# Kernel optimization log

Measured on AMD Instinct MI355X. Metric: run time of the kernel, lower is better.

## Reference

```python
import jax, jax.numpy as jnp
import numpy as np

B, T, C, M = 32, 720, 862, 4
PRED, LABEL = 720, 48
D, H, FF, LAYERS = 512, 8, 2048, 3
E = D // H
LN_EPS = 1e-5
REVIN_EPS = 1e-5


def _ln(x, w, b):
    mu = jnp.mean(x, axis=-1, keepdims=True)
    var = jnp.var(x, axis=-1, keepdims=True)
    return (x - mu) * jax.lax.rsqrt(var + LN_EPS) * w + b


def _flow_attention(q, k, v):
    # q, k, v: [B, H, L, E]. Flowformer: sigmoid kernel + flow conservation
    # (incoming/outgoing normalizers), competition (sigmoid) and allocation (softmax).
    q = jax.nn.sigmoid(q)
    k = jax.nn.sigmoid(k)
    eps = 1e-6
    Lq, Ls = q.shape[2], k.shape[2]
    nr = 1.0 / jnp.einsum('bhld,bhd->bhl', q + eps, k.sum(2) + eps)          # sink incoming
    nc = 1.0 / jnp.einsum('bhsd,bhd->bhs', k + eps, q.sum(2) + eps)          # source outgoing
    nr_ref = jnp.einsum('bhld,bhd->bhl', q + eps, (k * nc[..., None]).sum(2) + eps)
    nc_ref = jnp.einsum('bhsd,bhd->bhs', k + eps, (q * nr[..., None]).sum(2) + eps)
    nr_ref = jax.nn.sigmoid(nr_ref * (float(Lq) / float(Ls)))                # competition
    nc_ref = jax.nn.softmax(nc_ref, axis=-1) * Ls                            # allocation
    kv = jnp.einsum('bhse,bhsd->bhed', k, v * nc_ref[..., None])             # [B,H,E,E]
    return jnp.einsum('bhle,bhed->bhld', q, kv) * (nr * nr_ref)[..., None]


def _forward(x_enc, x_mark_enc, x_dec, revin_w, revin_b, emb_W, emb_b,
             Wq, bq, Wk, bk, Wv, bv, Wo, bo,
             ff1_W, ff1_b, ff2_W, ff2_b,
             ln1_w, ln1_b, ln2_w, ln2_b, lnf_w, lnf_b, proj_W, proj_b):
    # RevIN 'norm': per-channel instance norm over time + affine
    mean = jnp.mean(x_enc, axis=1, keepdims=True)
    stdev = jnp.sqrt(jnp.var(x_enc, axis=1, keepdims=True) + REVIN_EPS)
    xn = (x_enc - mean) / stdev * revin_w + revin_b
    # inverted embedding: each channel / covariate series -> one d_model token
    tok = jnp.concatenate([xn.transpose(0, 2, 1), x_mark_enc.transpose(0, 2, 1)], axis=1)  # [B, C+M, T]
    x = tok @ emb_W + emb_b  # [B, C+M, D]
    Ltok = x.shape[1]
    for l in range(LAYERS):
        q = (x @ Wq[l] + bq[l]).reshape(B, Ltok, H, E).transpose(0, 2, 1, 3)
        k = (x @ Wk[l] + bk[l]).reshape(B, Ltok, H, E).transpose(0, 2, 1, 3)
        v = (x @ Wv[l] + bv[l]).reshape(B, Ltok, H, E).transpose(0, 2, 1, 3)
        a = _flow_attention(q, k, v).transpose(0, 2, 1, 3).reshape(B, Ltok, D)
        x = _ln(x + (a @ Wo[l] + bo[l]), ln1_w[l], ln1_b[l])
        y = jax.nn.gelu(x @ ff1_W[l] + ff1_b[l], approximate=False)
        x = _ln(x + (y @ ff2_W[l] + ff2_b[l]), ln2_w[l], ln2_b[l])
    x = _ln(x, lnf_w, lnf_b)
    out = (x @ proj_W + proj_b).transpose(0, 2, 1)[:, :, :x_dec.shape[-1]]  # [B, PRED, C]
    # RevIN 'denorm'
    out = (out - revin_b) / (revin_w + REVIN_EPS * REVIN_EPS)
    out = out * stdev + mean
    return out[:, -PRED:, :]


def setup_inputs() -> dict:
    key = jax.random.key(0)
    ks = iter(jax.random.split(key, 40))

    def rn(shape, scale=0.02):
        return (jax.random.normal(next(ks), shape, jnp.float32) * scale)

    return {
        'x_enc': jax.random.normal(next(ks), (B, T, C), jnp.float32),
        'x_mark_enc': jax.random.normal(next(ks), (B, T, M), jnp.float32),
        'x_dec': jax.random.normal(next(ks), (B, LABEL + PRED, C), jnp.float32),
        'x_mark_dec': jax.random.normal(next(ks), (B, LABEL + PRED, M), jnp.float32),
        'revin_w': jnp.ones((C,), jnp.float32),
        'revin_b': jnp.zeros((C,), jnp.float32),
        'emb_W': rn((T, D)), 'emb_b': jnp.zeros((D,), jnp.float32),
        'Wq': rn((LAYERS, D, D)), 'bq': jnp.zeros((LAYERS, D), jnp.float32),
        'Wk': rn((LAYERS, D, D)), 'bk': jnp.zeros((LAYERS, D), jnp.float32),
        'Wv': rn((LAYERS, D, D)), 'bv': jnp.zeros((LAYERS, D), jnp.float32),
        'Wo': rn((LAYERS, D, D)), 'bo': jnp.zeros((LAYERS, D), jnp.float32),
        'ff1_W': rn((LAYERS, D, FF)), 'ff1_b': jnp.zeros((LAYERS, FF), jnp.float32),
        'ff2_W': rn((LAYERS, FF, D)), 'ff2_b': jnp.zeros((LAYERS, D), jnp.float32),
        'ln1_w': jnp.ones((LAYERS, D), jnp.float32), 'ln1_b': jnp.zeros((LAYERS, D), jnp.float32),
        'ln2_w': jnp.ones((LAYERS, D), jnp.float32), 'ln2_b': jnp.zeros((LAYERS, D), jnp.float32),
        'lnf_w': jnp.ones((D,), jnp.float32), 'lnf_b': jnp.zeros((D,), jnp.float32),
        'proj_W': rn((D, PRED)), 'proj_b': jnp.zeros((PRED,), jnp.float32),
    }


def reference(x_enc, x_mark_enc, x_dec, x_mark_dec, revin_w, revin_b, emb_W, emb_b,
              Wq, bq, Wk, bk, Wv, bv, Wo, bo,
              ff1_W, ff1_b, ff2_W, ff2_b,
              ln1_w, ln1_b, ln2_w, ln2_b, lnf_w, lnf_b, proj_W, proj_b):
    return _forward(x_enc, x_mark_enc, x_dec, revin_w, revin_b, emb_W, emb_b,
                    Wq, bq, Wk, bk, Wv, bv, Wo, bo,
                    ff1_W, ff1_b, ff2_W, ff2_b,
                    ln1_w, ln1_b, ln2_w, ln2_b, lnf_w, lnf_b, proj_W, proj_b)
```

## Files before the change

### kernel.cpp

```cpp
#include <hip/hip_runtime.h>
#include <math.h>

#define BB 32
#define TT 720
#define CC 862
#define MM 4
#define LTOK 866
#define DD 512
#define HH 8
#define EE 64
#define FFD 2048
#define NTOK (BB * LTOK)
#define NBH (BB * HH)
#define KPAD 736
#define NPADP 768
#define LSPLIT 4
#define LCHUNK 224
#define KVSPLIT 8
#define KVCHUNK 112
#define QS 1536
#define TSPL 8
#define TCH 90
#define CSLD 136

typedef unsigned short ushort_t;
typedef short s8v __attribute__((ext_vector_type(8)));
typedef float f4v __attribute__((ext_vector_type(4)));

__device__ __forceinline__ float wave_sum(float v) {
    #pragma unroll
    for (int off = 32; off; off >>= 1) v += __shfl_xor(v, off, 64);
    return v;
}
__device__ __forceinline__ float b2f(ushort_t u) {
    return __uint_as_float(((unsigned int)u) << 16);
}
__device__ __forceinline__ ushort_t f2b(float f) {
    unsigned int u = __float_as_uint(f);
    u = (u + 0x7FFFu + ((u >> 16) & 1u)) >> 16;
    return (ushort_t)u;
}

__device__ __forceinline__ void xcd_tile(int gx, int* m_t, int* n_t) {
    int nwg = gx * gridDim.y;
    int bid = blockIdx.y * gx + blockIdx.x;
    int xcd = bid & 7;
    int lid = bid >> 3;
    int q = nwg >> 3, r = nwg & 7;
    int wgid = (xcd < r ? xcd * (q + 1) : r * (q + 1) + (xcd - r) * q) + lid;
    *m_t = wgid / gx;
    *n_t = wgid % gx;
}

__global__ __launch_bounds__(256) void revin_part(const float* __restrict__ x_enc,
                                                  float* __restrict__ pS,
                                                  float* __restrict__ pS2) {
    int b = blockIdx.y, tz = blockIdx.z;
    int c = blockIdx.x * 64 + (threadIdx.x & 63);
    int g = threadIdx.x >> 6;
    float s = 0.f, s2 = 0.f;
    if (c < CC) {
        int t0 = tz * TCH;
        for (int t = t0 + g; t < t0 + TCH; t += 4) {
            float v = x_enc[((size_t)b * TT + t) * CC + c];
            s += v; s2 += v * v;
        }
    }
    __shared__ float ls[4][64], ls2[4][64];
    ls[g][threadIdx.x & 63] = s; ls2[g][threadIdx.x & 63] = s2;
    __syncthreads();
    if (g == 0 && c < CC) {
        int cx = threadIdx.x & 63;
        s = ls[0][cx] + ls[1][cx] + ls[2][cx] + ls[3][cx];
        s2 = ls2[0][cx] + ls2[1][cx] + ls2[2][cx] + ls2[3][cx];
        pS[((size_t)tz * BB + b) * CC + c] = s;
        pS2[((size_t)tz * BB + b) * CC + c] = s2;
    }
}

__global__ __launch_bounds__(256) void revin_fin(const float* __restrict__ pS,
                                                 const float* __restrict__ pS2,
                                                 float* __restrict__ mean,
                                                 float* __restrict__ stdev) {
    int idx = blockIdx.x * 256 + threadIdx.x;
    if (idx >= BB * CC) return;
    float s = 0.f, s2 = 0.f;
    #pragma unroll
    for (int tz = 0; tz < TSPL; tz++) {
        s += pS[(size_t)tz * BB * CC + idx];
        s2 += pS2[(size_t)tz * BB * CC + idx];
    }
    float mu = s / (float)TT;
    float var = s2 / (float)TT - mu * mu;
    mean[idx] = mu;
    stdev[idx] = sqrtf(var + 1e-5f);
}

__global__ __launch_bounds__(256) void build_tok(const float* __restrict__ x_enc,
                                                 const float* __restrict__ x_mark,
                                                 const float* __restrict__ mean,
                                                 const float* __restrict__ stdev,
                                                 const float* __restrict__ rw,
                                                 const float* __restrict__ rb,
                                                 ushort_t* __restrict__ tok) {
    int b = blockIdx.z;
    int r0 = blockIdx.x * 32, t0 = blockIdx.y * 32;
    __shared__ float tile[32][33];
    int tx = threadIdx.x & 31, ty = threadIdx.x >> 5;
    #pragma unroll
    for (int kk = 0; kk < 4; kk++) {
        int t = t0 + ty + kk * 8, r = r0 + tx;
        float v = 0.f;
        if (t < TT && r < LTOK) {
            if (r < CC) {
                float xv = x_enc[((size_t)b * TT + t) * CC + r];
                v = (xv - mean[b * CC + r]) / stdev[b * CC + r] * rw[r] + rb[r];
            } else {
                v = x_mark[((size_t)b * TT + t) * MM + (r - CC)];
            }
        }
        tile[ty + kk * 8][tx] = v;
    }
    __syncthreads();
    #pragma unroll
    for (int kk = 0; kk < 4; kk++) {
        int r = r0 + ty + kk * 8, t = t0 + tx;
        if (r < LTOK && t < KPAD)
            tok[((size_t)b * LTOK + r) * KPAD + t] = f2b(tile[tx][ty + kk * 8]);
    }
}

__global__ __launch_bounds__(256) void convT(const float* __restrict__ W,
                                             ushort_t* __restrict__ Wt,
                                             int K, int N, int KP, int NP) {
    __shared__ float tile[32][33];
    int k0 = blockIdx.x * 32, n0 = blockIdx.y * 32;
    int tx = threadIdx.x & 31, ty = threadIdx.x >> 5;
    #pragma unroll
    for (int r = 0; r < 4; r++) {
        int k = k0 + ty + r * 8, n = n0 + tx;
        tile[ty + r * 8][tx] = (k < K && n < N) ? W[(size_t)k * N + n] : 0.f;
    }
    __syncthreads();
    #pragma unroll
    for (int r = 0; r < 4; r++) {
        int n = n0 + ty + r * 8, k = k0 + tx;
        if (n < NP && k < KP)
            Wt[(size_t)n * KP + k] = f2b(tile[tx][ty + r * 8]);
    }
}

#define GLL(g, l) __builtin_amdgcn_global_load_lds( \
    (const __attribute__((address_space(1))) void*)(g), \
    (__attribute__((address_space(3))) void*)(l), 16, 0, 0)

template <int ACT, bool OF, bool OB>
__global__ __launch_bounds__(256) void bgemm(const ushort_t* __restrict__ A,
                                             const ushort_t* __restrict__ Bt,
                                             const float* __restrict__ bias,
                                             float* __restrict__ Cf,
                                             ushort_t* __restrict__ Cb,
                                             int Mdim, int Kdim, int Nout) {
    __shared__ ushort_t smem[17408];
    ushort_t* As = smem;
    ushort_t* Bs = smem + 4096;
    const int tid = threadIdx.x;
    const int lane = tid & 63;
    const int wid = tid >> 6;
    int m_t, n_t;
    xcd_tile(gridDim.x, &m_t, &n_t);
    const int m0 = m_t * 128;
    const int n0 = n_t * 128;
    const int wm = wid & 1, wn = wid >> 1;

    f4v acc[4][4];
    #pragma unroll
    for (int i = 0; i < 4; i++)
        #pragma unroll
        for (int j = 0; j < 4; j++)
            acc[i][j] = (f4v){0.f, 0.f, 0.f, 0.f};

    const int srow = wid * 16 + (lane >> 2);
    const int skq = ((lane & 3) ^ ((lane >> 3) & 3)) * 8;
    int ar0 = m0 + srow;       if (ar0 > Mdim - 1) ar0 = Mdim - 1;
    int ar1 = m0 + 64 + srow;  if (ar1 > Mdim - 1) ar1 = Mdim - 1;
    const ushort_t* gA0 = A + (size_t)ar0 * Kdim + skq;
    const ushort_t* gA1 = A + (size_t)ar1 * Kdim + skq;
    const ushort_t* gB0 = Bt + (size_t)(n0 + srow) * Kdim + skq;
    const ushort_t* gB1 = Bt + (size_t)(n0 + 64 + srow) * Kdim + skq;
    ushort_t* lA0 = As + (wid * 16) * 32;
    ushort_t* lA1 = As + (64 + wid * 16) * 32;
    ushort_t* lB0 = Bs + (wid * 16) * 32;
    ushort_t* lB1 = Bs + (64 + wid * 16) * 32;

    const int lr = lane & 15;
    const int kc = (((lane >> 4) ^ ((lane >> 1) & 3))) * 8;

    for (int k0 = 0; k0 < Kdim; k0 += 32) {
        GLL(gA0 + k0, lA0);
        GLL(gA1 + k0, lA1);
        GLL(gB0 + k0, lB0);
        GLL(gB1 + k0, lB1);
        __syncthreads();
        s8v af[4], bf[4];
        #pragma unroll
        for (int i = 0; i < 4; i++)
            af[i] = *(const s8v*)&As[(wm * 64 + i * 16 + lr) * 32 + kc];
        #pragma unroll
        for (int j = 0; j < 4; j++)
            bf[j] = *(const s8v*)&Bs[(wn * 64 + j * 16 + lr) * 32 + kc];
        #pragma unroll
        for (int i = 0; i < 4; i++)
            #pragma unroll
            for (int j = 0; j < 4; j++)
                acc[i][j] = __builtin_amdgcn_mfma_f32_16x16x32_bf16(af[i], bf[j], acc[i][j], 0, 0, 0);
        __syncthreads();
    }

    const int orow = (lane >> 4) * 4;
    if (OF) {
        #pragma unroll
        for (int j = 0; j < 4; j++) {
            int col = n0 + wn * 64 + j * 16 + lr;
            bool cok = col < Nout;
            float bb = cok ? bias[col] : 0.f;
            #pragma unroll
            for (int i = 0; i < 4; i++) {
                #pragma unroll
                for (int r = 0; r < 4; r++) {
                    int row = m0 + wm * 64 + i * 16 + orow + r;
                    if (cok && row < Mdim) {
                        float v = acc[i][j][r] + bb;
                        if (ACT == 1) v = 0.5f * v * (1.0f + erff(v * 0.70710678118654752f));
                        if (ACT == 2) v = 1.0f / (1.0f + expf(-v));
                        Cf[(size_t)row * Nout + col] = v;
                    }
                }
            }
        }
    }
    if (OB) {
        #pragma unroll
        for (int j = 0; j < 4; j++) {
            int cl = wn * 64 + j * 16 + lr;
            int gcol = n0 + cl;
            float bb = (gcol < Nout) ? bias[gcol] : 0.f;
            #pragma unroll
            for (int i = 0; i < 4; i++) {
                #pragma unroll
                for (int r = 0; r < 4; r++) {
                    float v = acc[i][j][r] + bb;
                    if (ACT == 1) v = 0.5f * v * (1.0f + erff(v * 0.70710678118654752f));
                    if (ACT == 2) v = 1.0f / (1.0f + expf(-v));
                    smem[(wm * 64 + i * 16 + orow + r) * CSLD + cl] = f2b(v);
                }
            }
        }
        __syncthreads();
        #pragma unroll
        for (int c = 0; c < 8; c++) {
            int idx = c * 256 + tid;
            int row = idx >> 4, cs = idx & 15;
            int grow = m0 + row, gcol = n0 + cs * 8;
            if (grow < Mdim) {
                if (gcol + 8 <= Nout) {
                    *(s8v*)&Cb[(size_t)grow * Nout + gcol] = *(const s8v*)&smem[row * CSLD + cs * 8];
                } else if (gcol < Nout) {
                    for (int q = 0; q < Nout - gcol; q++)
                        Cb[(size_t)grow * Nout + gcol + q] = smem[row * CSLD + cs * 8 + q];
                }
            }
        }
    }
}

__global__ __launch_bounds__(256) void bgemm_qkv(const ushort_t* __restrict__ A,
                                                 const ushort_t* __restrict__ Bt,
                                                 const float* __restrict__ bq_,
                                                 const float* __restrict__ bk_,
                                                 const float* __restrict__ bv_,
                                                 ushort_t* __restrict__ Cb,
                                                 int Mdim) {
    __shared__ ushort_t smem[17408];
    ushort_t* As = smem;
    ushort_t* Bs = smem + 4096;
    const int tid = threadIdx.x;
    const int lane = tid & 63;
    const int wid = tid >> 6;
    int m_t, n_t;
    xcd_tile(gridDim.x, &m_t, &n_t);
    const int m0 = m_t * 128;
    const int n0 = n_t * 128;
    const int wm = wid & 1, wn = wid >> 1;

    f4v acc[4][4];
    #pragma unroll
    for (int i = 0; i < 4; i++)
        #pragma unroll
        for (int j = 0; j < 4; j++)
            acc[i][j] = (f4v){0.f, 0.f, 0.f, 0.f};

    const int srow = wid * 16 + (lane >> 2);
    const int skq = ((lane & 3) ^ ((lane >> 3) & 3)) * 8;
    int ar0 = m0 + srow;       if (ar0 > Mdim - 1) ar0 = Mdim - 1;
    int ar1 = m0 + 64 + srow;  if (ar1 > Mdim - 1) ar1 = Mdim - 1;
    const ushort_t* gA0 = A + (size_t)ar0 * DD + skq;
    const ushort_t* gA1 = A + (size_t)ar1 * DD + skq;
    const ushort_t* gB0 = Bt + (size_t)(n0 + srow) * DD + skq;
    const ushort_t* gB1 = Bt + (size_t)(n0 + 64 + srow) * DD + skq;
    ushort_t* lA0 = As + (wid * 16) * 32;
    ushort_t* lA1 = As + (64 + wid * 16) * 32;
    ushort_t* lB0 = Bs + (wid * 16) * 32;
    ushort_t* lB1 = Bs + (64 + wid * 16) * 32;

    const int lr = lane & 15;
    const int kc = (((lane >> 4) ^ ((lane >> 1) & 3))) * 8;

    for (int k0 = 0; k0 < DD; k0 += 32) {
        GLL(gA0 + k0, lA0);
        GLL(gA1 + k0, lA1);
        GLL(gB0 + k0, lB0);
        GLL(gB1 + k0, lB1);
        __syncthreads();
        s8v af[4], bf[4];
        #pragma unroll
        for (int i = 0; i < 4; i++)
            af[i] = *(const s8v*)&As[(wm * 64 + i * 16 + lr) * 32 + kc];
        #pragma unroll
        for (int j = 0; j < 4; j++)
            bf[j] = *(const s8v*)&Bs[(wn * 64 + j * 16 + lr) * 32 + kc];
        #pragma unroll
        for (int i = 0; i < 4; i++)
            #pragma unroll
            for (int j = 0; j < 4; j++)
                acc[i][j] = __builtin_amdgcn_mfma_f32_16x16x32_bf16(af[i], bf[j], acc[i][j], 0, 0, 0);
        __syncthreads();
    }

    const int orow = (lane >> 4) * 4;
    #pragma unroll
    for (int j = 0; j < 4; j++) {
        int cl = wn * 64 + j * 16 + lr;
        int col = n0 + cl;
        int sec = col >> 9;
        const float* bsel = (sec == 0) ? bq_ : ((sec == 1) ? bk_ : bv_);
        float bb = bsel[col & 511];
        #pragma unroll
        for (int i = 0; i < 4; i++) {
            #pragma unroll
            for (int r = 0; r < 4; r++) {
                float v = acc[i][j][r] + bb;
                if (sec < 2) v = 1.0f / (1.0f + expf(-v));
                smem[(wm * 64 + i * 16 + orow + r) * CSLD + cl] = f2b(v);
            }
        }
    }
    __syncthreads();
    #pragma unroll
    for (int c = 0; c < 8; c++) {
        int idx = c * 256 + tid;
        int row = idx >> 4, cs = idx & 15;
        int grow = m0 + row;
        if (grow < Mdim)
            *(s8v*)&Cb[(size_t)grow * QS + n0 + cs * 8] = *(const s8v*)&smem[row * CSLD + cs * 8];
    }
}

__global__ __launch_bounds__(256) void ln_kernel(float* __restrict__ x,
                                                 const ushort_t* __restrict__ res,
                                                 const float* __restrict__ w,
                                                 const float* __restrict__ bp,
                                                 ushort_t* __restrict__ xb) {
    size_t base = (size_t)blockIdx.x * DD;
    int tid = threadIdx.x;
    float v0 = x[base + tid];
    float v1 = x[base + tid + 256];
    if (res != nullptr) { v0 += b2f(res[base + tid]); v1 += b2f(res[base + tid + 256]); }
    float s = wave_sum(v0 + v1);
    float s2 = wave_sum(v0 * v0 + v1 * v1);
    __shared__ float a1[4], a2[4];
    if ((tid & 63) == 0) { a1[tid >> 6] = s; a2[tid >> 6] = s2; }
    __syncthreads();
    s = a1[0] + a1[1] + a1[2] + a1[3];
    s2 = a2[0] + a2[1] + a2[2] + a2[3];
    float mu = s * (1.0f / DD);
    float var = s2 * (1.0f / DD) - mu * mu;
    float rs = rsqrtf(var + 1e-5f);
    float o0 = (v0 - mu) * rs * w[tid] + bp[tid];
    float o1 = (v1 - mu) * rs * w[tid + 256] + bp[tid + 256];
    x[base + tid] = o0;
    x[base + tid + 256] = o1;
    xb[base + tid] = f2b(o0);
    xb[base + tid + 256] = f2b(o1);
}

template <bool WEIGHTED>
__global__ __launch_bounds__(256) void attn_sums(const ushort_t* __restrict__ Q,
                                                 const ushort_t* __restrict__ Kp,
                                                 const float* __restrict__ wq,
                                                 const float* __restrict__ wk,
                                                 float* __restrict__ qsumP,
                                                 float* __restrict__ ksumP) {
    int bh = blockIdx.x;
    int sp = blockIdx.y;
    int b = bh >> 3, h = bh & 7;
    int lane = threadIdx.x & 63, g = threadIdx.x >> 6;
    int eo = (lane & 7) * 8;
    int lofs = lane >> 3;
    const size_t base = ((size_t)b * LTOK) * QS + h * 64 + eo;
    float aq[8] = {}, ak[8] = {};
    int lend = sp * LCHUNK + LCHUNK; if (lend > LTOK) lend = LTOK;
    for (int l = sp * LCHUNK + g * 8 + lofs; l < lend; l += 32) {
        s8v q8 = *(const s8v*)&Q[base + (size_t)l * QS];
        s8v k8 = *(const s8v*)&Kp[base + (size_t)l * QS];
        float wqv = 1.f, wkv = 1.f;
        if (WEIGHTED) { wqv = wq[bh * LTOK + l]; wkv = wk[bh * LTOK + l]; }
        #pragma unroll
        for (int j = 0; j < 8; j++) {
            aq[j] += b2f((ushort_t)q8[j]) * wqv;
            ak[j] += b2f((ushort_t)k8[j]) * wkv;
        }
    }
    #pragma unroll
    for (int off = 8; off < 64; off <<= 1) {
        #pragma unroll
        for (int j = 0; j < 8; j++) {
            aq[j] += __shfl_xor(aq[j], off, 64);
            ak[j] += __shfl_xor(ak[j], off, 64);
        }
    }
    __shared__ float sqs[4][64], sks[4][64];
    if (lofs == 0) {
        #pragma unroll
        for (int j = 0; j < 8; j++) { sqs[g][eo + j] = aq[j]; sks[g][eo + j] = ak[j]; }
    }
    __syncthreads();
    if (threadIdx.x < 64) {
        int e = threadIdx.x;
        float fq = sqs[0][e] + sqs[1][e] + sqs[2][e] + sqs[3][e];
        float fk = sks[0][e] + sks[1][e] + sks[2][e] + sks[3][e];
        qsumP[((size_t)sp * NBH + bh) * 64 + e] = fq;
        ksumP[((size_t)sp * NBH + bh) * 64 + e] = fk;
    }
}

template <int MODE>
__global__ __launch_bounds__(256) void attn_dots(const ushort_t* __restrict__ Q,
                                                 const ushort_t* __restrict__ Kp,
                                                 const float* __restrict__ Sq,
                                                 const float* __restrict__ Sk,
                                                 float* __restrict__ outq,
                                                 float* __restrict__ outk) {
    int bh = blockIdx.x;
    int b = bh >> 3, h = bh & 7;
    int lane = threadIdx.x & 63, w = threadIdx.x >> 6;
    float sq = 0.f, sk = 0.f;
    #pragma unroll
    for (int sp = 0; sp < LSPLIT; sp++) {
        sq += Sq[((size_t)sp * NBH + bh) * 64 + lane];
        sk += Sk[((size_t)sp * NBH + bh) * 64 + lane];
    }
    sq += 1e-6f; sk += 1e-6f;
    const size_t base = ((size_t)b * LTOK) * QS + h * 64 + lane;
    int l0 = blockIdx.y * 64 + w * 16;
    for (int i = 0; i < 16; i++) {
        int l = l0 + i;
        if (l >= LTOK) break;
        float dq = (b2f(Q[base + (size_t)l * QS]) + 1e-6f) * sq;
        float dk = (b2f(Kp[base + (size_t)l * QS]) + 1e-6f) * sk;
        dq = wave_sum(dq);
        dk = wave_sum(dk);
        if (lane == 0) {
            if (MODE == 0) { outq[bh * LTOK + l] = 1.0f / dq; outk[bh * LTOK + l] = 1.0f / dk; }
            else { outq[bh * LTOK + l] = 1.0f / (1.0f + expf(-dq)); outk[bh * LTOK + l] = dk; }
        }
    }
}

__global__ __launch_bounds__(256) void attn_softmax(float* __restrict__ buf) {
    float* p = buf + (size_t)blockIdx.x * LTOK;
    int tid = threadIdx.x;
    __shared__ float red[4];
    float mx = -1e30f;
    for (int l = tid; l < LTOK; l += 256) mx = fmaxf(mx, p[l]);
    #pragma unroll
    for (int off = 32; off; off >>= 1) mx = fmaxf(mx, __shfl_xor(mx, off, 64));
    if ((tid & 63) == 0) red[tid >> 6] = mx;
    __syncthreads();
    mx = fmaxf(fmaxf(red[0], red[1]), fmaxf(red[2], red[3]));
    __syncthreads();
    float s = 0.f;
    for (int l = tid; l < LTOK; l += 256) s += expf(p[l] - mx);
    s = wave_sum(s);
    if ((tid & 63) == 0) red[tid >> 6] = s;
    __syncthreads();
    s = red[0] + red[1] + red[2] + red[3];
    float scale = (float)LTOK / s;
    for (int l = tid; l < LTOK; l += 256) p[l] = expf(p[l] - mx) * scale;
}

__global__ __launch_bounds__(256) void attn_kv_part(const ushort_t* __restrict__ Kp,
                                                    const ushort_t* __restrict__ V,
                                                    const float* __restrict__ ncref,
                                                    float* __restrict__ kvpart) {
    int bh = blockIdx.x;
    int sp = blockIdx.y;
    int b = bh >> 3, h = bh & 7;
    int d = threadIdx.x & 63, eg = threadIdx.x >> 6;
    __shared__ float ks[16][64], vs[16][64];
    float acc[16] = {};
    const size_t base = ((size_t)b * LTOK) * QS + h * 64;
    const int s_begin = sp * KVCHUNK;
    int s_end = s_begin + KVCHUNK; if (s_end > LTOK) s_end = LTOK;

    const bool isV = threadIdx.x >= 128;
    const int slot = threadIdx.x & 127;
    const int srow = slot >> 3;
    const int e0 = (slot & 7) * 8;
    const ushort_t* src = isV ? V : Kp;

    for (int s0 = s_begin; s0 < s_end; s0 += 16) {
        __syncthreads();
        int s = s0 + srow;
        float vals[8] = {};
        if (s < s_end) {
            s8v raw = *(const s8v*)&src[base + (size_t)s * QS + e0];
            float mul = isV ? ncref[bh * LTOK + s] : 1.f;
            #pragma unroll
            for (int j = 0; j < 8; j++) vals[j] = b2f((ushort_t)raw[j]) * mul;
        }
        float (*dst)[64] = isV ? vs : ks;
        #pragma unroll
        for (int j = 0; j < 8; j++) dst[srow][e0 + j] = vals[j];
        __syncthreads();
        int nsi = s_end - s0; if (nsi > 16) nsi = 16;
        for (int si = 0; si < nsi; si++) {
            float vv = vs[si][d];
            #pragma unroll
            for (int i = 0; i < 16; i++) acc[i] += ks[si][eg * 16 + i] * vv;
        }
    }
    #pragma unroll
    for (int i = 0; i < 16; i++)
        kvpart[((size_t)sp * NBH + bh) * 4096 + (eg * 16 + i) * 64 + d] = acc[i];
}

__global__ __launch_bounds__(256) void kv_reduce(const float* __restrict__ part,
                                                 ushort_t* __restrict__ kvtb) {
    size_t idx = (size_t)blockIdx.x * 256 + threadIdx.x;
    float s = 0.f;
    #pragma unroll
    for (int sp = 0; sp < KVSPLIT; sp++)
        s += part[(size_t)sp * ((size_t)NBH * 4096) + idx];
    size_t bhbase = idx & ~(size_t)4095;
    int e = (int)((idx >> 6) & 63), d = (int)(idx & 63);
    kvtb[bhbase + (size_t)d * 64 + e] = f2b(s);
}

__global__ __launch_bounds__(256) void attn_out_mfma(const ushort_t* __restrict__ Q,
                                                     const ushort_t* __restrict__ kvtb,
                                                     const float* __restrict__ nr,
                                                     const float* __restrict__ nrref,
                                                     ushort_t* __restrict__ out) {
    int bh = blockIdx.x;
    int b = bh >> 3, h = bh & 7;
    const int lane = threadIdx.x & 63;
    const int wid = threadIdx.x >> 6;
    const int m0 = blockIdx.y * 256 + wid * 64;
    const int lr = lane & 15;
    const int kq = (lane >> 4) * 8;
    const size_t qbase = ((size_t)b * LTOK) * QS + h * 64;
    const size_t obase = ((size_t)b * LTOK) * DD + h * 64;

    s8v bf[2][4];
    #pragma unroll
    for (int ks = 0; ks < 2; ks++)
        #pragma unroll
        for (int j = 0; j < 4; j++)
            bf[ks][j] = *(const s8v*)&kvtb[(size_t)bh * 4096 + (size_t)(j * 16 + lr) * 64 + ks * 32 + kq];

    f4v acc[4][4];
    #pragma unroll
    for (int i = 0; i < 4; i++)
        #pragma unroll
        for (int j = 0; j < 4; j++)
            acc[i][j] = (f4v){0.f, 0.f, 0.f, 0.f};

    #pragma unroll
    for (int ks = 0; ks < 2; ks++) {
        #pragma unroll
        for (int i = 0; i < 4; i++) {
            int row = m0 + i * 16 + lr;
            if (row > LTOK - 1) row = LTOK - 1;
            s8v af = *(const s8v*)&Q[qbase + (size_t)row * QS + ks * 32 + kq];
            #pragma unroll
            for (int j = 0; j < 4; j++)
                acc[i][j] = __builtin_amdgcn_mfma_f32_16x16x32_bf16(af, bf[ks][j], acc[i][j], 0, 0, 0);
        }
    }

    const int orow = (lane >> 4) * 4;
    #pragma unroll
    for (int i = 0; i < 4; i++) {
        #pragma unroll
        for (int r = 0; r < 4; r++) {
            int l = m0 + i * 16 + orow + r;
            if (l >= LTOK) continue;
            float sc = nr[bh * LTOK + l] * nrref[bh * LTOK + l];
            #pragma unroll
            for (int j = 0; j < 4; j++) {
                int d = j * 16 + lr;
                out[obase + (size_t)l * DD + d] = f2b(acc[i][j][r] * sc);
            }
        }
    }
}

__global__ __launch_bounds__(256) void final_out(const ushort_t* __restrict__ p,
                                                 const float* __restrict__ mean,
                                                 const float* __restrict__ stdev,
                                                 const float* __restrict__ rw,
                                                 const float* __restrict__ rb,
                                                 float* __restrict__ out) {
    int b = blockIdx.z;
    int c0 = blockIdx.x * 32, t0 = blockIdx.y * 32;
    __shared__ float tile[32][33];
    int tx = threadIdx.x & 31, ty = threadIdx.x >> 5;
    #pragma unroll
    for (int kk = 0; kk < 4; kk++) {
        int c = c0 + ty + kk * 8, t = t0 + tx;
        float v = 0.f;
        if (c < CC && t < TT) v = b2f(p[((size_t)b * LTOK + c) * TT + t]);
        tile[ty + kk * 8][tx] = v;
    }
    __syncthreads();
    #pragma unroll
    for (int kk = 0; kk < 4; kk++) {
        int t = t0 + ty + kk * 8, c = c0 + tx;
        if (c < CC && t < TT) {
            float v = tile[tx][ty + kk * 8];
            v = (v - rb[c]) / (rw[c] + 1e-10f);
            v = v * stdev[b * CC + c] + mean[b * CC + c];
            out[((size_t)b * TT + t) * CC + c] = v;
        }
    }
}

extern "C" void kernel_launch(void* const* d_in, const int* in_sizes, int n_in,
                              void* d_out, int out_size, void* d_ws, size_t ws_size,
                              hipStream_t stream) {
    (void)in_sizes; (void)n_in; (void)out_size; (void)ws_size;
    const float* x_enc   = (const float*)d_in[0];
    const float* x_mark  = (const float*)d_in[1];
    const float* revin_w = (const float*)d_in[4];
    const float* revin_b = (const float*)d_in[5];
    const float* emb_W   = (const float*)d_in[6];
    const float* emb_b   = (const float*)d_in[7];
    const float* Wq = (const float*)d_in[8];
    const float* bq = (const float*)d_in[9];
    const float* Wk = (const float*)d_in[10];
    const float* bk = (const float*)d_in[11];
    const float* Wv = (const float*)d_in[12];
    const float* bv = (const float*)d_in[13];
    const float* Wo = (const float*)d_in[14];
    const float* bo = (const float*)d_in[15];
    const float* ff1_W = (const float*)d_in[16];
    const float* ff1_b = (const float*)d_in[17];
    const float* ff2_W = (const float*)d_in[18];
    const float* ff2_b = (const float*)d_in[19];
    const float* ln1_w = (const float*)d_in[20];
    const float* ln1_b = (const float*)d_in[21];
    const float* ln2_w = (const float*)d_in[22];
    const float* ln2_b = (const float*)d_in[23];
    const float* lnf_w = (const float*)d_in[24];
    const float* lnf_b = (const float*)d_in[25];
    const float* proj_W = (const float*)d_in[26];
    const float* proj_b = (const float*)d_in[27];
    float* out = (float*)d_out;

    char* wsb = (char*)d_ws;
    size_t off = 0;
    auto alloc = [&](size_t bytes) {
        off = (off + 63) & ~(size_t)63;
        void* p = wsb + off; off += bytes; return p;
    };
    float* mean  = (float*)alloc((size_t)BB * CC * 4);
    float* stdev = (float*)alloc((size_t)BB * CC * 4);
    float* pS    = (float*)alloc((size_t)TSPL * BB * CC * 4);
    float* pS2   = (float*)alloc((size_t)TSPL * BB * CC * 4);
    float* qsumP  = (float*)alloc((size_t)LSPLIT * NBH * 64 * 4);
    float* ksumP  = (float*)alloc((size_t)LSPLIT * NBH * 64 * 4);
    float* qnsumP = (float*)alloc((size_t)LSPLIT * NBH * 64 * 4);
    float* knsumP = (float*)alloc((size_t)LSPLIT * NBH * 64 * 4);
    float* nr    = (float*)alloc((size_t)NBH * LTOK * 4);
    float* nc    = (float*)alloc((size_t)NBH * LTOK * 4);
    float* nrref = (float*)alloc((size_t)NBH * LTOK * 4);
    float* ncref = (float*)alloc((size_t)NBH * LTOK * 4);
    ushort_t* kvtb = (ushort_t*)alloc((size_t)NBH * 4096 * 2);
    float* x     = (float*)alloc((size_t)NTOK * DD * 4);
    ushort_t* xb = (ushort_t*)alloc((size_t)NTOK * DD * 2);
    ushort_t* qkvb = (ushort_t*)alloc((size_t)NTOK * QS * 2);
    ushort_t* wbuf = (ushort_t*)alloc((size_t)10207232 * 2);
    ushort_t* U  = (ushort_t*)alloc((size_t)NTOK * KPAD * 2);

    ushort_t* embT = wbuf;
    ushort_t* qkvT = embT + (size_t)512 * KPAD;
    ushort_t* oT   = qkvT + (size_t)3 * 786432;
    ushort_t* f1T  = oT + 3 * 262144;
    ushort_t* f2T  = f1T + (size_t)3 * 1048576;
    ushort_t* pT   = f2T + (size_t)3 * 1048576;
    ushort_t* tokb  = U;
    ushort_t* ffb   = U;
    ushort_t* projb = U;
    float* kvpart   = (float*)U;
    ushort_t* ab    = U;
    ushort_t* tmpb  = qkvb;

    dim3 blk(256);
    auto cvt = [&](const float* W, ushort_t* Wt, int K, int N, int KP, int NP) {
        convT<<<dim3((KP + 31) / 32, (NP + 31) / 32), blk, 0, stream>>>(W, Wt, K, N, KP, NP);
    };
    cvt(emb_W, embT, TT, DD, KPAD, DD);
    for (int l = 0; l < 3; l++) {
        ushort_t* lb = qkvT + (size_t)l * 786432;
        cvt(Wq + (size_t)l * DD * DD, lb,          DD, DD, DD, DD);
        cvt(Wk + (size_t)l * DD * DD, lb + 262144, DD, DD, DD, DD);
        cvt(Wv + (size_t)l * DD * DD, lb + 524288, DD, DD, DD, DD);
        cvt(Wo + (size_t)l * DD * DD, oT + (size_t)l * 262144, DD, DD, DD, DD);
        cvt(ff1_W + (size_t)l * DD * FFD, f1T + (size_t)l * 1048576, DD, FFD, DD, FFD);
        cvt(ff2_W + (size_t)l * FFD * DD, f2T + (size_t)l * 1048576, FFD, DD, FFD, DD);
    }
    cvt(proj_W, pT, DD, TT, DD, NPADP);

    revin_part<<<dim3((CC + 63) / 64, BB, TSPL), blk, 0, stream>>>(x_enc, pS, pS2);
    revin_fin<<<dim3((BB * CC + 255) / 256), blk, 0, stream>>>(pS, pS2, mean, stdev);
    build_tok<<<dim3((LTOK + 31) / 32, (KPAD + 31) / 32, BB), blk, 0, stream>>>(
        x_enc, x_mark, mean, stdev, revin_w, revin_b, tokb);
    const int MT = (NTOK + 127) / 128;
    bgemm<0, true, true><<<dim3(DD / 128, MT), blk, 0, stream>>>(
        tokb, embT, emb_b, x, xb, NTOK, KPAD, DD);

    int ltiles = (LTOK + 63) / 64;
    for (int l = 0; l < 3; l++) {
        bgemm_qkv<<<dim3(QS / 128, MT), blk, 0, stream>>>(
            xb, qkvT + (size_t)l * 786432, bq + l * DD, bk + l * DD, bv + l * DD,
            qkvb, NTOK);
        attn_sums<false><<<dim3(NBH, LSPLIT), blk, 0, stream>>>(
            qkvb, qkvb + 512, nullptr, nullptr, qsumP, ksumP);
        attn_dots<0><<<dim3(NBH, ltiles), blk, 0, stream>>>(
            qkvb, qkvb + 512, ksumP, qsumP, nr, nc);
        attn_sums<true><<<dim3(NBH, LSPLIT), blk, 0, stream>>>(
            qkvb, qkvb + 512, nr, nc, qnsumP, knsumP);
        attn_dots<1><<<dim3(NBH, ltiles), blk, 0, stream>>>(
            qkvb, qkvb + 512, knsumP, qnsumP, nrref, ncref);
        attn_softmax<<<NBH, blk, 0, stream>>>(ncref);
        attn_kv_part<<<dim3(NBH, KVSPLIT), blk, 0, stream>>>(
            qkvb + 512, qkvb + 1024, ncref, kvpart);
        kv_reduce<<<dim3((NBH * 4096) / 256), blk, 0, stream>>>(kvpart, kvtb);
        attn_out_mfma<<<dim3(NBH, 4), blk, 0, stream>>>(qkvb, kvtb, nr, nrref, ab);
        bgemm<0, false, true><<<dim3(DD / 128, MT), blk, 0, stream>>>(
            ab, oT + (size_t)l * 262144, bo + l * DD, nullptr, tmpb, NTOK, DD, DD);
        ln_kernel<<<NTOK, blk, 0, stream>>>(x, tmpb, ln1_w + l * DD, ln1_b + l * DD, xb);
        for (int t0 = 0; t0 < NTOK / 64; t0 += 108) {
            int nt = NTOK / 64 - t0; if (nt > 108) nt = 108;
            int rs = t0 * 64, mc = nt * 64;
            bgemm<1, false, true><<<dim3(FFD / 128, (mc + 127) / 128), blk, 0, stream>>>(
                xb + (size_t)rs * DD, f1T + (size_t)l * 1048576, ff1_b + l * FFD,
                nullptr, ffb, mc, DD, FFD);
            bgemm<0, false, true><<<dim3(DD / 128, (mc + 127) / 128), blk, 0, stream>>>(
                ffb, f2T + (size_t)l * 1048576, ff2_b + l * DD,
                nullptr, tmpb + (size_t)rs * DD, mc, FFD, DD);
        }
        ln_kernel<<<NTOK, blk, 0, stream>>>(x, tmpb, ln2_w + l * DD, ln2_b + l * DD, xb);
    }
    ln_kernel<<<NTOK, blk, 0, stream>>>(x, nullptr, lnf_w, lnf_b, xb);
    bgemm<0, false, true><<<dim3(NPADP / 128, MT), blk, 0, stream>>>(
        xb, pT, proj_b, nullptr, projb, NTOK, DD, TT);
    final_out<<<dim3((CC + 31) / 32, (TT + 31) / 32, BB), blk, 0, stream>>>(
        projb, mean, stdev, revin_w, revin_b, out);
}
```

Before: 2.736 ms.

## Double-buffer LDS tiles in bf16 GEMM kernels to overlap loads with MFMA

Both the generic bf16 GEMM and the fused QKV GEMM now keep two LDS stages of A and B tiles. The global_load_lds for the next K-tile is issued right after the barrier, before the MFMA work on the current tile, so load latency can hide behind compute. This also drops the trailing barrier in each iteration, leaving one barrier per K step. A barrier is added before the epilogue reuses shared memory. The cost is twice the LDS used for staging, which still fits inside the existing shared array.

Result: faster. 2.443 ms (-10.7%).

```diff
diff --git a/kernel.cpp b/kernel.cpp
--- a/kernel.cpp
+++ b/kernel.cpp
@@ -162,8 +162,6 @@
                                              ushort_t* __restrict__ Cb,
                                              int Mdim, int Kdim, int Nout) {
     __shared__ ushort_t smem[17408];
-    ushort_t* As = smem;
-    ushort_t* Bs = smem + 4096;
     const int tid = threadIdx.x;
     const int lane = tid & 63;
     const int wid = tid >> 6;
@@ -188,34 +186,42 @@
     const ushort_t* gA1 = A + (size_t)ar1 * Kdim + skq;
     const ushort_t* gB0 = Bt + (size_t)(n0 + srow) * Kdim + skq;
     const ushort_t* gB1 = Bt + (size_t)(n0 + 64 + srow) * Kdim + skq;
-    ushort_t* lA0 = As + (wid * 16) * 32;
-    ushort_t* lA1 = As + (64 + wid * 16) * 32;
-    ushort_t* lB0 = Bs + (wid * 16) * 32;
-    ushort_t* lB1 = Bs + (64 + wid * 16) * 32;
+    const int aoff0 = (wid * 16) * 32;
+    const int aoff1 = (64 + wid * 16) * 32;
 
     const int lr = lane & 15;
     const int kc = (((lane >> 4) ^ ((lane >> 1) & 3))) * 8;
 
-    for (int k0 = 0; k0 < Kdim; k0 += 32) {
-        GLL(gA0 + k0, lA0);
-        GLL(gA1 + k0, lA1);
-        GLL(gB0 + k0, lB0);
-        GLL(gB1 + k0, lB1);
+    #define STAGE_T(k0v, boffv) do { \
+        GLL(gA0 + (k0v), smem + (boffv) + aoff0); \
+        GLL(gA1 + (k0v), smem + (boffv) + aoff1); \
+        GLL(gB0 + (k0v), smem + (boffv) + 4096 + aoff0); \
+        GLL(gB1 + (k0v), smem + (boffv) + 4096 + aoff1); \
+    } while (0)
+
+    const int nt = Kdim >> 5;
+    STAGE_T(0, 0);
+    int boff = 0;
+    for (int t = 0; t < nt; ++t) {
         __syncthreads();
+        if (t + 1 < nt) STAGE_T((t + 1) * 32, boff ^ 8192);
+        const ushort_t* Asr = smem + boff;
+        const ushort_t* Bsr = smem + boff + 4096;
         s8v af[4], bf[4];
         #pragma unroll
         for (int i = 0; i < 4; i++)
-            af[i] = *(const s8v*)&As[(wm * 64 + i * 16 + lr) * 32 + kc];
+            af[i] = *(const s8v*)&Asr[(wm * 64 + i * 16 + lr) * 32 + kc];
         #pragma unroll
         for (int j = 0; j < 4; j++)
-            bf[j] = *(const s8v*)&Bs[(wn * 64 + j * 16 + lr) * 32 + kc];
+            bf[j] = *(const s8v*)&Bsr[(wn * 64 + j * 16 + lr) * 32 + kc];
         #pragma unroll
         for (int i = 0; i < 4; i++)
             #pragma unroll
             for (int j = 0; j < 4; j++)
                 acc[i][j] = __builtin_amdgcn_mfma_f32_16x16x32_bf16(af[i], bf[j], acc[i][j], 0, 0, 0);
-        __syncthreads();
-    }
+        boff ^= 8192;
+    }
+    #undef STAGE_T
 
     const int orow = (lane >> 4) * 4;
     if (OF) {
@@ -240,6 +246,7 @@
         }
     }
     if (OB) {
+        __syncthreads();
         #pragma unroll
         for (int j = 0; j < 4; j++) {
             int cl = wn * 64 + j * 16 + lr;
@@ -282,8 +289,6 @@
                                                  ushort_t* __restrict__ Cb,
                                                  int Mdim) {
     __shared__ ushort_t smem[17408];
-    ushort_t* As = smem;
-    ushort_t* Bs = smem + 4096;
     const int tid = threadIdx.x;
     const int lane = tid & 63;
     const int wid = tid >> 6;
@@ -308,36 +313,45 @@
     const ushort_t* gA1 = A + (size_t)ar1 * DD + skq;
     const ushort_t* gB0 = Bt + (size_t)(n0 + srow) * DD + skq;
     const ushort_t* gB1 = Bt + (size_t)(n0 + 64 + srow) * DD + skq;
-    ushort_t* lA0 = As + (wid * 16) * 32;
-    ushort_t* lA1 = As + (64 + wid * 16) * 32;
-    ushort_t* lB0 = Bs + (wid * 16) * 32;
-    ushort_t* lB1 = Bs + (64 + wid * 16) * 32;
+    const int aoff0 = (wid * 16) * 32;
+    const int aoff1 = (64 + wid * 16) * 32;
 
     const int lr = lane & 15;
     const int kc = (((lane >> 4) ^ ((lane >> 1) & 3))) * 8;
 
-    for (int k0 = 0; k0 < DD; k0 += 32) {
-        GLL(gA0 + k0, lA0);
-        GLL(gA1 + k0, lA1);
-        GLL(gB0 + k0, lB0);
-        GLL(gB1 + k0, lB1);
+    #define STAGE_T(k0v, boffv) do { \
+        GLL(gA0 + (k0v), smem + (boffv) + aoff0); \
+        GLL(gA1 + (k0v), smem + (boffv) + aoff1); \
+        GLL(gB0 + (k0v), smem + (boffv) + 4096 + aoff0); \
+        GLL(gB1 + (k0v), smem + (boffv) + 4096 + aoff1); \
+    } while (0)
+
+    const int nt = DD >> 5;
+    STAGE_T(0, 0);
+    int boff = 0;
+    for (int t = 0; t < nt; ++t) {
         __syncthreads();
+        if (t + 1 < nt) STAGE_T((t + 1) * 32, boff ^ 8192);
+        const ushort_t* Asr = smem + boff;
+        const ushort_t* Bsr = smem + boff + 4096;
         s8v af[4], bf[4];
         #pragma unroll
         for (int i = 0; i < 4; i++)
-            af[i] = *(const s8v*)&As[(wm * 64 + i * 16 + lr) * 32 + kc];
+            af[i] = *(const s8v*)&Asr[(wm * 64 + i * 16 + lr) * 32 + kc];
         #pragma unroll
         for (int j = 0; j < 4; j++)
-            bf[j] = *(const s8v*)&Bs[(wn * 64 + j * 16 + lr) * 32 + kc];
+            bf[j] = *(const s8v*)&Bsr[(wn * 64 + j * 16 + lr) * 32 + kc];
         #pragma unroll
         for (int i = 0; i < 4; i++)
             #pragma unroll
             for (int j = 0; j < 4; j++)
                 acc[i][j] = __builtin_amdgcn_mfma_f32_16x16x32_bf16(af[i], bf[j], acc[i][j], 0, 0, 0);
-        __syncthreads();
-    }
+        boff ^= 8192;
+    }
+    #undef STAGE_T
 
     const int orow = (lane >> 4) * 4;
+    __syncthreads();
     #pragma unroll
     for (int j = 0; j < 4; j++) {
         int cl = wn * 64 + j * 16 + lr;
```

## Double-buffer LDS tiles in bf16 GEMMs to overlap global loads with MFMA

Applied to the files above, without the earlier changes.

The bgemm and bgemm_qkv main loops now use two LDS stages. The next K-slice is issued through global_load_lds right after a single barrier, so it loads while MFMAs run on the current slice, and the second barrier per iteration is gone. To keep LDS at 32KB, the bf16 epilogue now writes the output tile in two 64-row halves through the shared buffer instead of all 128 rows at once. This adds epilogue barriers, and correctness depends on the async LDS loads being complete at the following barrier.

Result: faster. 2.656 ms (-2.9%).

```diff
diff --git a/kernel.cpp b/kernel.cpp
--- a/kernel.cpp
+++ b/kernel.cpp
@@ -161,9 +161,7 @@
                                              float* __restrict__ Cf,
                                              ushort_t* __restrict__ Cb,
                                              int Mdim, int Kdim, int Nout) {
-    __shared__ ushort_t smem[17408];
-    ushort_t* As = smem;
-    ushort_t* Bs = smem + 4096;
+    __shared__ ushort_t smem[16384];
     const int tid = threadIdx.x;
     const int lane = tid & 63;
     const int wid = tid >> 6;
@@ -188,34 +186,47 @@
     const ushort_t* gA1 = A + (size_t)ar1 * Kdim + skq;
     const ushort_t* gB0 = Bt + (size_t)(n0 + srow) * Kdim + skq;
     const ushort_t* gB1 = Bt + (size_t)(n0 + 64 + srow) * Kdim + skq;
-    ushort_t* lA0 = As + (wid * 16) * 32;
-    ushort_t* lA1 = As + (64 + wid * 16) * 32;
-    ushort_t* lB0 = Bs + (wid * 16) * 32;
-    ushort_t* lB1 = Bs + (64 + wid * 16) * 32;
+    const int aoff = wid * 512;
 
     const int lr = lane & 15;
     const int kc = (((lane >> 4) ^ ((lane >> 1) & 3))) * 8;
 
-    for (int k0 = 0; k0 < Kdim; k0 += 32) {
-        GLL(gA0 + k0, lA0);
-        GLL(gA1 + k0, lA1);
-        GLL(gB0 + k0, lB0);
-        GLL(gB1 + k0, lB1);
-        __syncthreads();
-        s8v af[4], bf[4];
-        #pragma unroll
-        for (int i = 0; i < 4; i++)
-            af[i] = *(const s8v*)&As[(wm * 64 + i * 16 + lr) * 32 + kc];
-        #pragma unroll
-        for (int j = 0; j < 4; j++)
-            bf[j] = *(const s8v*)&Bs[(wn * 64 + j * 16 + lr) * 32 + kc];
-        #pragma unroll
-        for (int i = 0; i < 4; i++)
-            #pragma unroll
-            for (int j = 0; j < 4; j++)
-                acc[i][j] = __builtin_amdgcn_mfma_f32_16x16x32_bf16(af[i], bf[j], acc[i][j], 0, 0, 0);
-        __syncthreads();
-    }
+    #define STG(k0v, base) do { \
+        GLL(gA0 + (k0v), smem + (base) + aoff); \
+        GLL(gA1 + (k0v), smem + (base) + 2048 + aoff); \
+        GLL(gB0 + (k0v), smem + (base) + 4096 + aoff); \
+        GLL(gB1 + (k0v), smem + (base) + 4096 + 2048 + aoff); \
+    } while (0)
+
+    #define ITER(tv, curb, nxtb) do { \
+        __syncthreads(); \
+        if ((tv) + 1 < nt) STG(((tv) + 1) * 32, nxtb); \
+        const ushort_t* Asr = smem + (curb); \
+        const ushort_t* Bsr = smem + (curb) + 4096; \
+        s8v af[4], bf[4]; \
+        _Pragma("unroll") \
+        for (int i = 0; i < 4; i++) \
+            af[i] = *(const s8v*)&Asr[(wm * 64 + i * 16 + lr) * 32 + kc]; \
+        _Pragma("unroll") \
+        for (int j = 0; j < 4; j++) \
+            bf[j] = *(const s8v*)&Bsr[(wn * 64 + j * 16 + lr) * 32 + kc]; \
+        _Pragma("unroll") \
+        for (int i = 0; i < 4; i++) \
+            _Pragma("unroll") \
+            for (int j = 0; j < 4; j++) \
+                acc[i][j] = __builtin_amdgcn_mfma_f32_16x16x32_bf16(af[i], bf[j], acc[i][j], 0, 0, 0); \
+    } while (0)
+
+    const int nt = Kdim >> 5;
+    STG(0, 0);
+    int t = 0;
+    for (; t + 2 <= nt; t += 2) {
+        ITER(t, 0, 8192);
+        ITER(t + 1, 8192, 0);
+    }
+    if (t < nt) ITER(t, 0, 8192);
+    #undef ITER
+    #undef STG
 
     const int orow = (lane >> 4) * 4;
     if (OF) {
@@ -241,33 +252,39 @@
     }
     if (OB) {
         #pragma unroll
-        for (int j = 0; j < 4; j++) {
-            int cl = wn * 64 + j * 16 + lr;
-            int gcol = n0 + cl;
-            float bb = (gcol < Nout) ? bias[gcol] : 0.f;
-            #pragma unroll
-            for (int i = 0; i < 4; i++) {
+        for (int h = 0; h < 2; h++) {
+            __syncthreads();
+            if (wm == h) {
                 #pragma unroll
-                for (int r = 0; r < 4; r++) {
-                    float v = acc[i][j][r] + bb;
-                    if (ACT == 1) v = 0.5f * v * (1.0f + erff(v * 0.70710678118654752f));
-                    if (ACT == 2) v = 1.0f / (1.0f + expf(-v));
-                    smem[(wm * 64 + i * 16 + orow + r) * CSLD + cl] = f2b(v);
+                for (int j = 0; j < 4; j++) {
+                    int cl = wn * 64 + j * 16 + lr;
+                    int gcol = n0 + cl;
+                    float bb = (gcol < Nout) ? bias[gcol] : 0.f;
+                    #pragma unroll
+                    for (int i = 0; i < 4; i++) {
+                        #pragma unroll
+                        for (int r = 0; r < 4; r++) {
+                            float v = acc[i][j][r] + bb;
+                            if (ACT == 1) v = 0.5f * v * (1.0f + erff(v * 0.70710678118654752f));
+                            if (ACT == 2) v = 1.0f / (1.0f + expf(-v));
+                            smem[(i * 16 + orow + r) * CSLD + cl] = f2b(v);
+                        }
+                    }
                 }
             }
-        }
-        __syncthreads();
-        #pragma unroll
-        for (int c = 0; c < 8; c++) {
-            int idx = c * 256 + tid;
-            int row = idx >> 4, cs = idx & 15;
-            int grow = m0 + row, gcol = n0 + cs * 8;
-            if (grow < Mdim) {
-                if (gcol + 8 <= Nout) {
-                    *(s8v*)&Cb[(size_t)grow * Nout + gcol] = *(const s8v*)&smem[row * CSLD + cs * 8];
-                } else if (gcol < Nout) {
-                    for (int q = 0; q < Nout - gcol; q++)
-                        Cb[(size_t)grow * Nout + gcol + q] = smem[row * CSLD + cs * 8 + q];
+            __syncthreads();
+            #pragma unroll
+            for (int c = 0; c < 4; c++) {
+                int idx = c * 256 + tid;
+                int row = idx >> 4, cs = idx & 15;
+                int grow = m0 + h * 64 + row, gcol = n0 + cs * 8;
+                if (grow < Mdim) {
+                    if (gcol + 8 <= Nout) {
+                        *(s8v*)&Cb[(size_t)grow * Nout + gcol] = *(const s8v*)&smem[row * CSLD + cs * 8];
+                    } else if (gcol < Nout) {
+                        for (int q = 0; q < Nout - gcol; q++)
+                            Cb[(size_t)grow * Nout + gcol + q] = smem[row * CSLD + cs * 8 + q];
+                    }
                 }
             }
         }
@@ -281,9 +298,7 @@
                                                  const float* __restrict__ bv_,
                                                  ushort_t* __restrict__ Cb,
                                                  int Mdim) {
-    __shared__ ushort_t smem[17408];
-    ushort_t* As = smem;
-    ushort_t* Bs = smem + 4096;
+    __shared__ ushort_t smem[16384];
     const int tid = threadIdx.x;
     const int lane = tid & 63;
     const int wid = tid >> 6;
@@ -308,61 +323,78 @@
     const ushort_t* gA1 = A + (size_t)ar1 * DD + skq;
     const ushort_t* gB0 = Bt + (size_t)(n0 + srow) * DD + skq;
     const ushort_t* gB1 = Bt + (size_t)(n0 + 64 + srow) * DD + skq;
-    ushort_t* lA0 = As + (wid * 16) * 32;
-    ushort_t* lA1 = As + (64 + wid * 16) * 32;
-    ushort_t* lB0 = Bs + (wid * 16) * 32;
-    ushort_t* lB1 = Bs + (64 + wid * 16) * 32;
+    const int aoff = wid * 512;
 
     const int lr = lane & 15;
     const int kc = (((lane >> 4) ^ ((lane >> 1) & 3))) * 8;
 
-    for (int k0 = 0; k0 < DD; k0 += 32) {
-        GLL(gA0 + k0, lA0);
-        GLL(gA1 + k0, lA1);
-        GLL(gB0 + k0, lB0);
-        GLL(gB1 + k0, lB1);
+    #define STG(k0v, base) do { \
+        GLL(gA0 + (k0v), smem + (base) + aoff); \
+        GLL(gA1 + (k0v), smem + (base) + 2048 + aoff); \
+        GLL(gB0 + (k0v), smem + (base) + 4096 + aoff); \
+        GLL(gB1 + (k0v), smem + (base) + 4096 + 2048 + aoff); \
+    } while (0)
+
+    #define ITER(tv, curb, nxtb) do { \
+        __syncthreads(); \
+        if ((tv) + 1 < nt) STG(((tv) + 1) * 32, nxtb); \
+        const ushort_t* Asr = smem + (curb); \
+        const ushort_t* Bsr = smem + (curb) + 4096; \
+        s8v af[4], bf[4]; \
+        _Pragma("unroll") \
+        for (int i = 0; i < 4; i++) \
+            af[i] = *(const s8v*)&Asr[(wm * 64 + i * 16 + lr) * 32 + kc]; \
+        _Pragma("unroll") \
+        for (int j = 0; j < 4; j++) \
+            bf[j] = *(const s8v*)&Bsr[(wn * 64 + j * 16 + lr) * 32 + kc]; \
+        _Pragma("unroll") \
+        for (int i = 0; i < 4; i++) \
+            _Pragma("unroll") \
+            for (int j = 0; j < 4; j++) \
+                acc[i][j] = __builtin_amdgcn_mfma_f32_16x16x32_bf16(af[i], bf[j], acc[i][j], 0, 0, 0); \
+    } while (0)
+
+    const int nt = DD >> 5;
+    STG(0, 0);
+    for (int t = 0; t < nt; t += 2) {
+        ITER(t, 0, 8192);
+        ITER(t + 1, 8192, 0);
+    }
+    #undef ITER
+    #undef STG
+
+    const int orow = (lane >> 4) * 4;
+    #pragma unroll
+    for (int h = 0; h < 2; h++) {
         __syncthreads();
-        s8v af[4], bf[4];
-        #pragma unroll
-        for (int i = 0; i < 4; i++)
-            af[i] = *(const s8v*)&As[(wm * 64 + i * 16 + lr) * 32 + kc];
-        #pragma unroll
-        for (int j = 0; j < 4; j++)
-            bf[j] = *(const s8v*)&Bs[(wn * 64 + j * 16 + lr) * 32 + kc];
-        #pragma unroll
-        for (int i = 0; i < 4; i++)
+        if (wm == h) {
             #pragma unroll
-            for (int j = 0; j < 4; j++)
-                acc[i][j] = __builtin_amdgcn_mfma_f32_16x16x32_bf16(af[i], bf[j], acc[i][j], 0, 0, 0);
+            for (int j = 0; j < 4; j++) {
+                int cl = wn * 64 + j * 16 + lr;
+                int col = n0 + cl;
+                int sec = col >> 9;
+                const float* bsel = (sec == 0) ? bq_ : ((sec == 1) ? bk_ : bv_);
+                float bb = bsel[col & 511];
+                #pragma unroll
+                for (int i = 0; i < 4; i++) {
+                    #pragma unroll
+                    for (int r = 0; r < 4; r++) {
+                        float v = acc[i][j][r] + bb;
+                        if (sec < 2) v = 1.0f / (1.0f + expf(-v));
+                        smem[(i * 16 + orow + r) * CSLD + cl] = f2b(v);
+                    }
+                }
+            }
+        }
         __syncthreads();
-    }
-
-    const int orow = (lane >> 4) * 4;
-    #pragma unroll
-    for (int j = 0; j < 4; j++) {
-        int cl = wn * 64 + j * 16 + lr;
-        int col = n0 + cl;
-        int sec = col >> 9;
-        const float* bsel = (sec == 0) ? bq_ : ((sec == 1) ? bk_ : bv_);
-        float bb = bsel[col & 511];
-        #pragma unroll
-        for (int i = 0; i < 4; i++) {
-            #pragma unroll
-            for (int r = 0; r < 4; r++) {
-                float v = acc[i][j][r] + bb;
-                if (sec < 2) v = 1.0f / (1.0f + expf(-v));
-                smem[(wm * 64 + i * 16 + orow + r) * CSLD + cl] = f2b(v);
-            }
-        }
-    }
-    __syncthreads();
-    #pragma unroll
-    for (int c = 0; c < 8; c++) {
-        int idx = c * 256 + tid;
-        int row = idx >> 4, cs = idx & 15;
-        int grow = m0 + row;
-        if (grow < Mdim)
-            *(s8v*)&Cb[(size_t)grow * QS + n0 + cs * 8] = *(const s8v*)&smem[row * CSLD + cs * 8];
+        #pragma unroll
+        for (int c = 0; c < 4; c++) {
+            int idx = c * 256 + tid;
+            int row = idx >> 4, cs = idx & 15;
+            int grow = m0 + h * 64 + row;
+            if (grow < Mdim)
+                *(s8v*)&Cb[(size_t)grow * QS + n0 + cs * 8] = *(const s8v*)&smem[row * CSLD + cs * 8];
+        }
     }
 }
 
```
